# Kernel optimization log

Measured on AMD Instinct MI355X. Metric: run time of the kernel, lower is better.

The kernel has to match this reference:

```python
import jax, jax.numpy as jnp
import numpy as np

N_HEAD = 16
LORA_SCALE = 1.0 / 4.0  # alpha=1, r=4
LN_EPS = 1e-5


def _ln(x, g, b):
    # LayerNorm subclass casts to float32 then back to input dtype
    xf = x.astype(jnp.float32)
    m = xf.mean(-1, keepdims=True)
    v = xf.var(-1, keepdims=True)
    y = (xf - m) / jnp.sqrt(v + LN_EPS) * g + b
    return y.astype(x.dtype)


def _lora(h, a, b):
    # x @ a.T @ b.T * scaling ; a:[r,d], b:[d,r]
    return (h @ a.T) @ b.T * LORA_SCALE


def _attn(h, Wq, bq, Wk, Wv, bv, Wo, bo, la_k, lb_k, la_v, lb_v, la_o, lb_o):
    B, S, D = h.shape
    hd = D // N_HEAD
    scale = hd ** (-0.25)
    q = h @ Wq.T + bq
    k = h @ Wk.T + _lora(h, la_k, lb_k)          # key Linear has no bias
    v = h @ Wv.T + bv + _lora(h, la_v, lb_v)
    qh = q.reshape(B, S, N_HEAD, hd).transpose(0, 2, 1, 3) * scale  # [B,H,S,hd]
    kh = k.reshape(B, S, N_HEAD, hd).transpose(0, 2, 1, 3) * scale
    vh = v.reshape(B, S, N_HEAD, hd).transpose(0, 2, 1, 3)
    qk = jnp.einsum('bhqd,bhkd->bhqk', qh, kh).astype(jnp.float32)
    w = jax.nn.softmax(qk, axis=-1).astype(q.dtype)
    wv = jnp.einsum('bhqk,bhkd->bhqd', w, vh)
    wv = wv.transpose(0, 2, 1, 3).reshape(B, S, D)
    return wv @ Wo.T + bo + _lora(wv, la_o, lb_o)


def setup_inputs() -> dict:
    key = jax.random.key(0)
    D, R = 1024, 4
    B, S = 8, 1024
    ks = jax.random.split(key, 20)
    sd = 0.02
    inp = {
        'x': jax.random.normal(ks[0], (B, S, D), jnp.float32),
        'Wq': jax.random.normal(ks[1], (D, D), jnp.float32) * sd,
        'bq': jnp.zeros((D,), jnp.float32),
        'Wk': jax.random.normal(ks[2], (D, D), jnp.float32) * sd,
        'Wv': jax.random.normal(ks[3], (D, D), jnp.float32) * sd,
        'bv': jnp.zeros((D,), jnp.float32),
        'Wo': jax.random.normal(ks[4], (D, D), jnp.float32) * sd,
        'bo': jnp.zeros((D,), jnp.float32),
        'la_k': jax.random.normal(ks[5], (R, D), jnp.float32) * sd,
        'lb_k': jax.random.normal(ks[6], (D, R), jnp.float32) * sd,
        'la_v': jax.random.normal(ks[7], (R, D), jnp.float32) * sd,
        'lb_v': jax.random.normal(ks[8], (D, R), jnp.float32) * sd,
        'la_o': jax.random.normal(ks[9], (R, D), jnp.float32) * sd,
        'lb_o': jax.random.normal(ks[10], (D, R), jnp.float32) * sd,
        'g_attn': jnp.ones((D,), jnp.float32),
        'b_attn': jnp.zeros((D,), jnp.float32),
        'W1': jax.random.normal(ks[11], (4 * D, D), jnp.float32) * sd,
        'b1': jnp.zeros((4 * D,), jnp.float32),
        'W2': jax.random.normal(ks[12], (D, 4 * D), jnp.float32) * sd,
        'b2': jnp.zeros((D,), jnp.float32),
        'g_mlp': jnp.ones((D,), jnp.float32),
        'b_mlp': jnp.zeros((D,), jnp.float32),
    }
    return inp


def reference(x, Wq, bq, Wk, Wv, bv, Wo, bo, la_k, lb_k, la_v, lb_v, la_o, lb_o,
              g_attn, b_attn, W1, b1, W2, b2, g_mlp, b_mlp):
    # self-attention + residual (LoRA on key/value/out)
    x = x + _attn(_ln(x, g_attn, b_attn), Wq, bq, Wk, Wv, bv, Wo, bo,
                  la_k, lb_k, la_v, lb_v, la_o, lb_o)
    # MLP + residual (exact GELU, matching nn.GELU default)
    h = _ln(x, g_mlp, b_mlp)
    h = jax.nn.gelu(h @ W1.T + b1, approximate=False)
    x = x + h @ W2.T + b2
    return x
```

## Files before the change

kernel.cpp:

```cpp
#include <hip/hip_runtime.h>
#include <math.h>

typedef _Float16 f16_t;
typedef f16_t f16x8 __attribute__((ext_vector_type(8)));
typedef f16_t f16x4 __attribute__((ext_vector_type(4)));
typedef float f32x4 __attribute__((ext_vector_type(4)));
typedef float fv4 __attribute__((ext_vector_type(4)));

#define MFMA16(a, b, c) __builtin_amdgcn_mfma_f32_16x16x32_f16(a, b, c, 0, 0, 0)

__device__ __forceinline__ void gload16(const void* g, void* l) {
  __builtin_amdgcn_global_load_lds((const __attribute__((address_space(1))) void*)g,
                                   (__attribute__((address_space(3))) void*)l, 16, 0, 0);
}

__global__ __launch_bounds__(256) void ln_f32(const float* __restrict__ x,
                                              const float* __restrict__ g,
                                              const float* __restrict__ b,
                                              f16_t* __restrict__ y) {
  const int D = 1024;
  int row = blockIdx.x;
  int t = threadIdx.x;
  const float* xr = x + (size_t)row * D + t * 4;
  float x0 = xr[0], x1 = xr[1], x2 = xr[2], x3 = xr[3];
  float sum = x0 + x1 + x2 + x3;
  float sq = x0 * x0 + x1 * x1 + x2 * x2 + x3 * x3;
  for (int d = 32; d; d >>= 1) {
    sum += __shfl_down(sum, d);
    sq += __shfl_down(sq, d);
  }
  __shared__ float ssum[4], ssq[4];
  int w = t >> 6, lane = t & 63;
  if (lane == 0) { ssum[w] = sum; ssq[w] = sq; }
  __syncthreads();
  float ts = ssum[0] + ssum[1] + ssum[2] + ssum[3];
  float tq = ssq[0] + ssq[1] + ssq[2] + ssq[3];
  float mean = ts * (1.0f / 1024.0f);
  float var = tq * (1.0f / 1024.0f) - mean * mean;
  float rstd = rsqrtf(var + 1e-5f);
  f16_t* yr = y + (size_t)row * D + t * 4;
  const float* gr = g + t * 4;
  const float* br = b + t * 4;
  yr[0] = (f16_t)((x0 - mean) * rstd * gr[0] + br[0]);
  yr[1] = (f16_t)((x1 - mean) * rstd * gr[1] + br[1]);
  yr[2] = (f16_t)((x2 - mean) * rstd * gr[2] + br[2]);
  yr[3] = (f16_t)((x3 - mean) * rstd * gr[3] + br[3]);
}

__global__ __launch_bounds__(256) void ln_f16(const f16_t* __restrict__ x,
                                              const float* __restrict__ g,
                                              const float* __restrict__ b,
                                              f16_t* __restrict__ y) {
  const int D = 1024;
  int row = blockIdx.x;
  int t = threadIdx.x;
  const f16_t* xr = x + (size_t)row * D + t * 4;
  float x0 = (float)xr[0], x1 = (float)xr[1], x2 = (float)xr[2], x3 = (float)xr[3];
  float sum = x0 + x1 + x2 + x3;
  float sq = x0 * x0 + x1 * x1 + x2 * x2 + x3 * x3;
  for (int d = 32; d; d >>= 1) {
    sum += __shfl_down(sum, d);
    sq += __shfl_down(sq, d);
  }
  __shared__ float ssum[4], ssq[4];
  int w = t >> 6, lane = t & 63;
  if (lane == 0) { ssum[w] = sum; ssq[w] = sq; }
  __syncthreads();
  float ts = ssum[0] + ssum[1] + ssum[2] + ssum[3];
  float tq = ssq[0] + ssq[1] + ssq[2] + ssq[3];
  float mean = ts * (1.0f / 1024.0f);
  float var = tq * (1.0f / 1024.0f) - mean * mean;
  float rstd = rsqrtf(var + 1e-5f);
  f16_t* yr = y + (size_t)row * D + t * 4;
  const float* gr = g + t * 4;
  const float* br = b + t * 4;
  yr[0] = (f16_t)((x0 - mean) * rstd * gr[0] + br[0]);
  yr[1] = (f16_t)((x1 - mean) * rstd * gr[1] + br[1]);
  yr[2] = (f16_t)((x2 - mean) * rstd * gr[2] + br[2]);
  yr[3] = (f16_t)((x3 - mean) * rstd * gr[3] + br[3]);
}

__global__ __launch_bounds__(256) void convert_w(
    const float* __restrict__ wq, const float* __restrict__ wk,
    const float* __restrict__ wv, const float* __restrict__ wo,
    const float* __restrict__ w1, const float* __restrict__ w2,
    f16_t* __restrict__ oq, f16_t* __restrict__ ok, f16_t* __restrict__ ov,
    f16_t* __restrict__ oo, f16_t* __restrict__ o1, f16_t* __restrict__ o2) {
  int bid = blockIdx.x;
  const float* src;
  f16_t* dst;
  int bi;
  if (bid < 2048) {
    int seg = bid >> 9;
    bi = bid & 511;
    src = seg == 0 ? wq : seg == 1 ? wk : seg == 2 ? wv : wo;
    dst = seg == 0 ? oq : seg == 1 ? ok : seg == 2 ? ov : oo;
  } else if (bid < 4096) {
    bi = bid - 2048; src = w1; dst = o1;
  } else {
    bi = bid - 4096; src = w2; dst = o2;
  }
  size_t idx = (size_t)bi * 2048 + (size_t)threadIdx.x * 8;
  fv4 a = *(const fv4*)(src + idx);
  fv4 b = *(const fv4*)(src + idx + 4);
  f16x8 h;
#pragma unroll
  for (int j = 0; j < 4; ++j) { h[j] = (f16_t)a[j]; h[4 + j] = (f16_t)b[j]; }
  *(f16x8*)(dst + idx) = h;
}

__global__ __launch_bounds__(256) void lora_kv_kernel(
    const f16_t* __restrict__ h, const float* __restrict__ la_k,
    const float* __restrict__ la_v, float* __restrict__ t_k,
    float* __restrict__ t_v, int K) {
  int lane = threadIdx.x & 63;
  int w = threadIdx.x >> 6;
  int row = blockIdx.x * 4 + w;
  const f16_t* hrow = h + (size_t)row * K;
  float ak[4] = {0.f, 0.f, 0.f, 0.f};
  float av[4] = {0.f, 0.f, 0.f, 0.f};
  for (int it = 0; it < K / 512; ++it) {
    int base = it * 512 + lane * 8;
    f16x8 hx = *(const f16x8*)(hrow + base);
#pragma unroll
    for (int r = 0; r < 4; ++r) {
      const float* kr = la_k + (size_t)r * K + base;
      const float* vr = la_v + (size_t)r * K + base;
#pragma unroll
      for (int j = 0; j < 8; ++j) {
        float hv = (float)hx[j];
        ak[r] += hv * kr[j];
        av[r] += hv * vr[j];
      }
    }
  }
#pragma unroll
  for (int r = 0; r < 4; ++r) {
    for (int d = 32; d; d >>= 1) {
      ak[r] += __shfl_down(ak[r], d);
      av[r] += __shfl_down(av[r], d);
    }
  }
  if (lane == 0) {
#pragma unroll
    for (int r = 0; r < 4; ++r) {
      t_k[(size_t)row * 4 + r] = ak[r];
      t_v[(size_t)row * 4 + r] = av[r];
    }
  }
}

__global__ __launch_bounds__(256) void lora_t_kernel(const f16_t* __restrict__ h,
                                                     const float* __restrict__ la,
                                                     float* __restrict__ t, int K) {
  int lane = threadIdx.x & 63;
  int w = threadIdx.x >> 6;
  int row = blockIdx.x * 4 + w;
  const f16_t* hrow = h + (size_t)row * K;
  float acc[4] = {0.f, 0.f, 0.f, 0.f};
  for (int it = 0; it < K / 512; ++it) {
    int base = it * 512 + lane * 8;
    f16x8 hx = *(const f16x8*)(hrow + base);
#pragma unroll
    for (int r = 0; r < 4; ++r) {
      const float* ar = la + (size_t)r * K + base;
#pragma unroll
      for (int j = 0; j < 8; ++j) acc[r] += (float)hx[j] * ar[j];
    }
  }
#pragma unroll
  for (int r = 0; r < 4; ++r) {
    for (int d = 32; d; d >>= 1) acc[r] += __shfl_down(acc[r], d);
  }
  if (lane == 0) {
#pragma unroll
    for (int r = 0; r < 4; ++r) t[(size_t)row * 4 + r] = acc[r];
  }
}

#define GEMM_PIPE_BODY                                                        \
  f32x4 acc[4][4];                                                            \
  _Pragma("unroll") for (int i = 0; i < 4; ++i)                               \
      _Pragma("unroll") for (int j = 0; j < 4; ++j)                           \
          acc[i][j] = (f32x4){0.f, 0.f, 0.f, 0.f};                            \
  const int nsteps = K >> 6;                                                  \
  stageA(0, 0); stageB(0, 0);                                                 \
  stageA(1, 1); stageB(1, 1);                                                 \
  stageA(2, 2); stageB(2, 2);                                                 \
  int b3 = 0;                                                                 \
  for (int kt = 0; kt < nsteps; ++kt) {                                       \
    if (kt + 2 < nsteps)                                                      \
      asm volatile("s_waitcnt vmcnt(12)" ::: "memory");                       \
    else if (kt + 1 < nsteps)                                                 \
      asm volatile("s_waitcnt vmcnt(6)" ::: "memory");                        \
    else                                                                      \
      asm volatile("s_waitcnt vmcnt(0)" ::: "memory");                        \
    __builtin_amdgcn_sched_barrier(0);                                        \
    __builtin_amdgcn_s_barrier();                                             \
    f16x8 af[4][2], bf[4][2];                                                 \
    _Pragma("unroll") for (int kk = 0; kk < 2; ++kk) {                        \
      _Pragma("unroll") for (int i = 0; i < 4; ++i) {                         \
        int row = wm * 64 + i * 16 + l15;                                     \
        af[i][kk] = *(const f16x8*)((const char*)Abuf[b3] + row * 128 +       \
                                    ((kk * 64 + lhi * 16) ^ ((row & 7) << 4)));\
      }                                                                       \
      _Pragma("unroll") for (int j = 0; j < 4; ++j) {                         \
        int row = wn * 64 + j * 16 + l15;                                     \
        bf[j][kk] = *(const f16x8*)((const char*)Bbuf[b3] + row * 128 +       \
                                    ((kk * 64 + lhi * 16) ^ ((row & 7) << 4)));\
      }                                                                       \
    }                                                                         \
    asm volatile("s_waitcnt lgkmcnt(0)" ::: "memory");                        \
    __builtin_amdgcn_sched_barrier(0);                                        \
    __builtin_amdgcn_s_barrier();                                             \
    if (kt + 3 < nsteps) { stageA(kt + 3, b3); stageB(kt + 3, b3); }          \
    __builtin_amdgcn_sched_barrier(0);                                        \
    __builtin_amdgcn_s_setprio(1);                                            \
    _Pragma("unroll") for (int kk = 0; kk < 2; ++kk)                          \
        _Pragma("unroll") for (int i = 0; i < 4; ++i)                         \
            _Pragma("unroll") for (int j = 0; j < 4; ++j)                     \
                acc[i][j] = MFMA16(af[i][kk], bf[j][kk], acc[i][j]);          \
    __builtin_amdgcn_s_setprio(0);                                            \
    b3 = (b3 == 2) ? 0 : b3 + 1;                                              \
  }

__global__ __launch_bounds__(512, 2) void gemm_pipe(
    const f16_t* __restrict__ A, const f16_t* __restrict__ B,
    const float* __restrict__ bias, const float* __restrict__ loraT,
    const float* __restrict__ loraB, const float* residf,
    const f16_t* __restrict__ residb, f16_t* Cb, float* Cf,
    int M, int N, int K, int ldb, int dogelu) {
  __shared__ __align__(16) f16_t Abuf[3][8192];
  __shared__ __align__(16) f16_t Bbuf[3][16384];
  const int tid = threadIdx.x;
  const int lane = tid & 63, wid = tid >> 6;
  const int wm = wid >> 2, wn = wid & 3;
  const int l15 = lane & 15, lhi = lane >> 4;
  int nwg = gridDim.x * gridDim.y;
  int bid = blockIdx.y * gridDim.x + blockIdx.x;
  int swz = (bid & 7) * (nwg >> 3) + (bid >> 3);
  const int m0 = (swz / gridDim.x) * 128, n0 = (swz % gridDim.x) * 256;
  const int arow = tid >> 3;
  const int aslot = tid & 7;

  auto stageA = [&](int step, int buf) {
#pragma unroll
    for (int c = 0; c < 2; ++c) {
      int r = c * 64 + arow;
      int cm = aslot ^ (r & 7);
      gload16(A + (size_t)(m0 + r) * K + (size_t)step * 64 + cm * 8,
              (char*)Abuf[buf] + c * 8192 + wid * 1024);
    }
  };
  auto stageB = [&](int step, int buf) {
#pragma unroll
    for (int c = 0; c < 4; ++c) {
      int r = c * 64 + arow;
      int cm = aslot ^ (r & 7);
      gload16(B + (size_t)(n0 + r) * ldb + (size_t)step * 64 + cm * 8,
              (char*)Bbuf[buf] + c * 8192 + wid * 1024);
    }
  };

  GEMM_PIPE_BODY

  const int gm = m0 + wm * 64, gn = n0 + wn * 64;
#pragma unroll
  for (int j = 0; j < 4; ++j) {
    int gcol = gn + j * 16 + l15;
    float bj = bias ? bias[gcol] : 0.f;
    float lb0 = 0.f, lb1 = 0.f, lb2 = 0.f, lb3 = 0.f;
    if (loraB) {
      const float* p = loraB + (size_t)gcol * 4;
      lb0 = p[0]; lb1 = p[1]; lb2 = p[2]; lb3 = p[3];
    }
#pragma unroll
    for (int i = 0; i < 4; ++i) {
      float v4[4];
#pragma unroll
      for (int r = 0; r < 4; ++r) {
        int grow = gm + i * 16 + lhi * 4 + r;
        float val = acc[i][j][r] + bj;
        if (loraT) {
          const float* tp = loraT + (size_t)grow * 4;
          val += 0.25f * (tp[0] * lb0 + tp[1] * lb1 + tp[2] * lb2 + tp[3] * lb3);
        }
        if (dogelu) val = 0.5f * val * (1.0f + erff(val * 0.70710678118654752f));
        if (residf) val += residf[(size_t)grow * N + gcol];
        if (residb) val += (float)residb[(size_t)grow * N + gcol];
        v4[r] = val;
      }
      if (Cf) {
#pragma unroll
        for (int r = 0; r < 4; ++r)
          Cf[(size_t)(gm + i * 16 + lhi * 4 + r) * N + gcol] = v4[r];
      } else {
#pragma unroll
        for (int r = 0; r < 4; ++r)
          Cb[(size_t)(gm + i * 16 + lhi * 4 + r) * N + gcol] = (f16_t)v4[r];
      }
    }
  }
}

__global__ __launch_bounds__(512, 2) void gemm_qkv_pipe(
    const f16_t* __restrict__ A, const f16_t* __restrict__ W,
    const float* __restrict__ bq, const float* __restrict__ bv,
    const float* __restrict__ t_k, const float* __restrict__ lb_k,
    const float* __restrict__ t_v, const float* __restrict__ lb_v,
    f16_t* __restrict__ Pq, f16_t* __restrict__ Pk, f16_t* __restrict__ Pvt,
    int K) {
  const int D = 1024;
  __shared__ __align__(16) f16_t Abuf[3][8192];
  __shared__ __align__(16) f16_t Bbuf[3][16384];
  const int tid = threadIdx.x;
  const int lane = tid & 63, wid = tid >> 6;
  const int wm = wid >> 2, wn = wid & 3;
  const int l15 = lane & 15, lhi = lane >> 4;
  int nwg = gridDim.x * gridDim.y;
  int bid = blockIdx.y * gridDim.x + blockIdx.x;
  int swz = (bid & 7) * (nwg >> 3) + (bid >> 3);
  const int m0 = (swz / gridDim.x) * 128, n0 = (swz % gridDim.x) * 256;
  const int seg = n0 >> 10;
  const int arow = tid >> 3;
  const int aslot = tid & 7;

  auto stageA = [&](int step, int buf) {
#pragma unroll
    for (int c = 0; c < 2; ++c) {
      int r = c * 64 + arow;
      int cm = aslot ^ (r & 7);
      gload16(A + (size_t)(m0 + r) * K + (size_t)step * 64 + cm * 8,
              (char*)Abuf[buf] + c * 8192 + wid * 1024);
    }
  };
  auto stageB = [&](int step, int buf) {
#pragma unroll
    for (int c = 0; c < 4; ++c) {
      int r = c * 64 + arow;
      int cm = aslot ^ (r & 7);
      gload16(W + (size_t)(n0 + r) * K + (size_t)step * 64 + cm * 8,
              (char*)Bbuf[buf] + c * 8192 + wid * 1024);
    }
  };

  GEMM_PIPE_BODY

  const int gm = m0 + wm * 64, gn = n0 + wn * 64;
  const float* tB = (seg == 1) ? t_k : t_v;
#pragma unroll
  for (int j = 0; j < 4; ++j) {
    int gcol = gn + j * 16 + l15;
    int c = gcol & 1023;
    float bj = (seg == 0) ? bq[c] : (seg == 2 ? bv[c] : 0.f);
    float lb0 = 0.f, lb1 = 0.f, lb2 = 0.f, lb3 = 0.f;
    if (seg) {
      const float* p = (seg == 1 ? lb_k : lb_v) + (size_t)c * 4;
      lb0 = p[0]; lb1 = p[1]; lb2 = p[2]; lb3 = p[3];
    }
#pragma unroll
    for (int i = 0; i < 4; ++i) {
      float v4[4];
#pragma unroll
      for (int r = 0; r < 4; ++r) {
        int grow = gm + i * 16 + lhi * 4 + r;
        float val = acc[i][j][r] + bj;
        if (seg) {
          const float* tp = tB + (size_t)grow * 4;
          val += 0.25f * (tp[0] * lb0 + tp[1] * lb1 + tp[2] * lb2 + tp[3] * lb3);
        }
        v4[r] = val;
      }
      if (seg < 2) {
        f16_t* dst = (seg == 0) ? Pq : Pk;
#pragma unroll
        for (int r = 0; r < 4; ++r)
          dst[(size_t)(gm + i * 16 + lhi * 4 + r) * D + c] = (f16_t)v4[r];
      } else {
        int grow0 = gm + i * 16 + lhi * 4;
        int bb = grow0 >> 10, ss = grow0 & 1023;
        int hh = c >> 6, dd = c & 63;
        f16x4 pk;
#pragma unroll
        for (int r = 0; r < 4; ++r) pk[r] = (f16_t)v4[r];
        *(f16x4*)(Pvt + (((size_t)bb * 16 + hh) * 64 + dd) * 1024 + ss) = pk;
      }
    }
  }
}

__global__ __launch_bounds__(256, 2) void gemm_mfma(
    const f16_t* __restrict__ A, const float* __restrict__ B,
    const float* __restrict__ bias, const float* __restrict__ loraT,
    const float* __restrict__ loraB, const float* residf,
    const f16_t* __restrict__ residb, f16_t* Cb, float* Cf, f16_t* Cvt,
    int M, int N, int K, int ldb, int dogelu) {
  __shared__ __align__(16) f16_t smem[2][16384];
  const int tid = threadIdx.x;
  const int lane = tid & 63, wid = tid >> 6;
  const int wm = wid >> 1, wn = wid & 1;
  const int l15 = lane & 15, lhi = lane >> 4;
  const int m0 = blockIdx.y * 128, n0 = blockIdx.x * 128;
  const int arow = tid >> 3;
  const int aslot = tid & 7;

  f32x4 acc[4][4];
#pragma unroll
  for (int i = 0; i < 4; ++i)
#pragma unroll
    for (int j = 0; j < 4; ++j) acc[i][j] = (f32x4){0.f, 0.f, 0.f, 0.f};

  fv4 breg[4][2];

  auto stageA = [&](int step, int buf) {
#pragma unroll
    for (int c = 0; c < 4; ++c) {
      int r = c * 32 + arow;
      int cm = aslot ^ (r & 7);
      gload16(A + (size_t)(m0 + r) * K + (size_t)step * 64 + cm * 8,
              (char*)&smem[buf][0] + c * 4096 + wid * 1024);
    }
  };
  auto loadB = [&](int step) {
#pragma unroll
    for (int c = 0; c < 4; ++c) {
      int r = c * 32 + arow;
      const float* gp = B + (size_t)(n0 + r) * ldb + (size_t)step * 64 + aslot * 8;
      breg[c][0] = *(const fv4*)gp;
      breg[c][1] = *(const fv4*)(gp + 4);
    }
  };
  auto writeB = [&](int buf) {
#pragma unroll
    for (int c = 0; c < 4; ++c) {
      int r = c * 32 + arow;
      f16x8 hh;
#pragma unroll
      for (int j = 0; j < 4; ++j) hh[j] = (f16_t)breg[c][0][j];
#pragma unroll
      for (int j = 0; j < 4; ++j) hh[4 + j] = (f16_t)breg[c][1][j];
      int boff = r * 128 + ((aslot * 16) ^ ((r & 7) << 4));
      *(f16x8*)((char*)&smem[buf][8192] + boff) = hh;
    }
  };

  const int nsteps = K >> 6;
  stageA(0, 0);
  loadB(0);
  writeB(0);
  __syncthreads();
  for (int t = 0; t < nsteps; ++t) {
    int cur = t & 1, nxt = cur ^ 1;
    if (t + 1 < nsteps) { stageA(t + 1, nxt); loadB(t + 1); }
    const char* As = (const char*)&smem[cur][0];
    const char* Bs = (const char*)&smem[cur][8192];
#pragma unroll
    for (int kk = 0; kk < 2; ++kk) {
      f16x8 af[4], bf[4];
#pragma unroll
      for (int i = 0; i < 4; ++i) {
        int row = wm * 64 + i * 16 + l15;
        af[i] = *(const f16x8*)(As + row * 128 + ((kk * 64 + lhi * 16) ^ ((row & 7) << 4)));
      }
#pragma unroll
      for (int j = 0; j < 4; ++j) {
        int row = wn * 64 + j * 16 + l15;
        bf[j] = *(const f16x8*)(Bs + row * 128 + ((kk * 64 + lhi * 16) ^ ((row & 7) << 4)));
      }
#pragma unroll
      for (int i = 0; i < 4; ++i)
#pragma unroll
        for (int j = 0; j < 4; ++j) acc[i][j] = MFMA16(af[i], bf[j], acc[i][j]);
    }
    if (t + 1 < nsteps) writeB(nxt);
    __syncthreads();
  }

  const int gm = m0 + wm * 64, gn = n0 + wn * 64;
#pragma unroll
  for (int j = 0; j < 4; ++j) {
    int gcol = gn + j * 16 + l15;
    float bj = bias ? bias[gcol] : 0.f;
    float lb0 = 0.f, lb1 = 0.f, lb2 = 0.f, lb3 = 0.f;
    if (loraB) {
      const float* p = loraB + (size_t)gcol * 4;
      lb0 = p[0]; lb1 = p[1]; lb2 = p[2]; lb3 = p[3];
    }
#pragma unroll
    for (int i = 0; i < 4; ++i) {
      float v4[4];
#pragma unroll
      for (int r = 0; r < 4; ++r) {
        int grow = gm + i * 16 + lhi * 4 + r;
        float val = acc[i][j][r] + bj;
        if (loraT) {
          const float* tp = loraT + (size_t)grow * 4;
          val += 0.25f * (tp[0] * lb0 + tp[1] * lb1 + tp[2] * lb2 + tp[3] * lb3);
        }
        if (dogelu) val = 0.5f * val * (1.0f + erff(val * 0.70710678118654752f));
        if (residf) val += residf[(size_t)grow * N + gcol];
        if (residb) val += (float)residb[(size_t)grow * N + gcol];
        v4[r] = val;
      }
      if (Cf) {
#pragma unroll
        for (int r = 0; r < 4; ++r)
          Cf[(size_t)(gm + i * 16 + lhi * 4 + r) * N + gcol] = v4[r];
      } else if (Cvt) {
        int grow0 = gm + i * 16 + lhi * 4;
        int bb = grow0 >> 10, ss = grow0 & 1023;
        int hh = gcol >> 6, dd = gcol & 63;
        f16x4 pk;
#pragma unroll
        for (int r = 0; r < 4; ++r) pk[r] = (f16_t)v4[r];
        *(f16x4*)(Cvt + (((size_t)bb * 16 + hh) * 64 + dd) * 1024 + ss) = pk;
      } else {
#pragma unroll
        for (int r = 0; r < 4; ++r)
          Cb[(size_t)(gm + i * 16 + lhi * 4 + r) * N + gcol] = (f16_t)v4[r];
      }
    }
  }
}

__global__ __launch_bounds__(256, 3) void attn_mfma(const f16_t* __restrict__ q,
                                                    const f16_t* __restrict__ k,
                                                    const f16_t* __restrict__ vt,
                                                    f16_t* __restrict__ wv) {
  const int S = 1024, D = 1024;
  __shared__ __align__(16) f16_t Qs[128 * 64];
  __shared__ __align__(16) f16_t SP[128 * 64];
  __shared__ __align__(16) f16_t Ks[64 * 64];
  __shared__ __align__(16) f16_t Vts[64 * 64];
  __shared__ float rsb[128];
  __shared__ float lib[128];
  const int tid = threadIdx.x, lane = tid & 63, w = tid >> 6;
  const int l15 = lane & 15, lhi = lane >> 4;
  const int q0 = blockIdx.x * 128;
  const int h = blockIdx.y, b = blockIdx.z;
  const f16_t* qg = q + ((size_t)b * S + q0) * D + h * 64;
  const f16_t* kg = k + (size_t)b * S * D + h * 64;
  const f16_t* vg = vt + ((size_t)b * 16 + h) * 64 * (size_t)S;

#pragma unroll
  for (int c = 0; c < 4; ++c) {
    int r = c * 32 + (tid >> 3), kc = tid & 7;
    f16x8 xx = *(const f16x8*)(qg + (size_t)r * D + kc * 8);
    *(f16x8*)((char*)Qs + r * 128 + ((kc * 16) ^ ((r & 7) << 4))) = xx;
  }
  __syncthreads();
  f16x8 qf[2][2];
#pragma unroll
  for (int i = 0; i < 2; ++i) {
    int row = w * 32 + i * 16 + l15;
#pragma unroll
    for (int kk = 0; kk < 2; ++kk)
      qf[i][kk] = *(const f16x8*)((char*)Qs + row * 128 +
                                  ((kk * 64 + lhi * 16) ^ ((row & 7) << 4)));
  }

  f32x4 oacc[2][4];
#pragma unroll
  for (int i = 0; i < 2; ++i)
#pragma unroll
    for (int j = 0; j < 4; ++j) oacc[i][j] = (f32x4){0.f, 0.f, 0.f, 0.f};
  float m_run = -1e30f, l_run = 0.f;
  const int myrow = w * 32 + (lane >> 1);
  const int half = lane & 1;

  for (int kv = 0; kv < 16; ++kv) {
    __syncthreads();
#pragma unroll
    for (int c = 0; c < 2; ++c) {
      int r = c * 32 + (tid >> 3), kc = tid & 7;
      f16x8 xk = *(const f16x8*)(kg + (size_t)(kv * 64 + r) * D + kc * 8);
      *(f16x8*)((char*)Ks + r * 128 + ((kc * 16) ^ ((r & 7) << 4))) = xk;
      f16x8 xv = *(const f16x8*)(vg + (size_t)r * S + kv * 64 + kc * 8);
      *(f16x8*)((char*)Vts + r * 128 + ((kc * 16) ^ ((r & 7) << 4))) = xv;
    }
    __syncthreads();
    f32x4 sacc[2][4];
#pragma unroll
    for (int i = 0; i < 2; ++i)
#pragma unroll
      for (int j = 0; j < 4; ++j) sacc[i][j] = (f32x4){0.f, 0.f, 0.f, 0.f};
#pragma unroll
    for (int kk = 0; kk < 2; ++kk) {
      f16x8 kf[4];
#pragma unroll
      for (int j = 0; j < 4; ++j) {
        int row = j * 16 + l15;
        kf[j] = *(const f16x8*)((char*)Ks + row * 128 +
                                ((kk * 64 + lhi * 16) ^ ((row & 7) << 4)));
      }
#pragma unroll
      for (int i = 0; i < 2; ++i)
#pragma unroll
        for (int j = 0; j < 4; ++j) sacc[i][j] = MFMA16(qf[i][kk], kf[j], sacc[i][j]);
    }
#pragma unroll
    for (int i = 0; i < 2; ++i)
#pragma unroll
      for (int j = 0; j < 4; ++j)
#pragma unroll
        for (int r = 0; r < 4; ++r) {
          int srow = w * 32 + i * 16 + lhi * 4 + r;
          int scol = j * 16 + l15;
          *(f16_t*)((char*)SP + srow * 128 + ((scol * 2) ^ ((srow & 7) << 4))) =
              (f16_t)(sacc[i][j][r] * 0.125f);
        }
    __syncthreads();
    f16x8 ch[4];
#pragma unroll
    for (int c = 0; c < 4; ++c)
      ch[c] = *(const f16x8*)((char*)SP + myrow * 128 +
                              ((half * 64 + c * 16) ^ ((myrow & 7) << 4)));
    float mt = -1e30f;
#pragma unroll
    for (int c = 0; c < 4; ++c)
#pragma unroll
      for (int e = 0; e < 8; ++e) mt = fmaxf(mt, (float)ch[c][e]);
    mt = fmaxf(mt, __shfl_xor(mt, 1));
    float mnew = fmaxf(m_run, mt);
    float resc = __expf(m_run - mnew);
    float lsum = 0.f;
#pragma unroll
    for (int c = 0; c < 4; ++c) {
      f16x8 p8;
#pragma unroll
      for (int e = 0; e < 8; ++e) {
        float p = __expf((float)ch[c][e] - mnew);
        lsum += p;
        p8[e] = (f16_t)p;
      }
      *(f16x8*)((char*)SP + myrow * 128 + ((half * 64 + c * 16) ^ ((myrow & 7) << 4))) = p8;
    }
    lsum += __shfl_xor(lsum, 1);
    l_run = l_run * resc + lsum;
    m_run = mnew;
    if (half == 0) rsb[myrow] = resc;
    __syncthreads();
#pragma unroll
    for (int i = 0; i < 2; ++i) {
      float f0 = rsb[w * 32 + i * 16 + lhi * 4 + 0];
      float f1 = rsb[w * 32 + i * 16 + lhi * 4 + 1];
      float f2 = rsb[w * 32 + i * 16 + lhi * 4 + 2];
      float f3 = rsb[w * 32 + i * 16 + lhi * 4 + 3];
#pragma unroll
      for (int j = 0; j < 4; ++j) {
        oacc[i][j][0] *= f0;
        oacc[i][j][1] *= f1;
        oacc[i][j][2] *= f2;
        oacc[i][j][3] *= f3;
      }
    }
#pragma unroll
    for (int kk = 0; kk < 2; ++kk) {
      f16x8 pa[2], vb[4];
#pragma unroll
      for (int i = 0; i < 2; ++i) {
        int row = w * 32 + i * 16 + l15;
        pa[i] = *(const f16x8*)((char*)SP + row * 128 +
                                ((kk * 64 + lhi * 16) ^ ((row & 7) << 4)));
      }
#pragma unroll
      for (int j = 0; j < 4; ++j) {
        int row = j * 16 + l15;
        vb[j] = *(const f16x8*)((char*)Vts + row * 128 +
                                ((kk * 64 + lhi * 16) ^ ((row & 7) << 4)));
      }
#pragma unroll
      for (int i = 0; i < 2; ++i)
#pragma unroll
        for (int j = 0; j < 4; ++j) oacc[i][j] = MFMA16(pa[i], vb[j], oacc[i][j]);
    }
  }
  if (half == 0) lib[myrow] = 1.f / l_run;
  __syncthreads();
#pragma unroll
  for (int i = 0; i < 2; ++i)
#pragma unroll
    for (int r = 0; r < 4; ++r) {
      int row = w * 32 + i * 16 + lhi * 4 + r;
      float li = lib[row];
      size_t base = ((size_t)b * S + q0 + row) * D + h * 64;
#pragma unroll
      for (int j = 0; j < 4; ++j)
        wv[base + j * 16 + l15] = (f16_t)(oacc[i][j][r] * li);
    }
}

extern "C" void kernel_launch(void* const* d_in, const int* in_sizes, int n_in,
                              void* d_out, int out_size, void* d_ws, size_t ws_size,
                              hipStream_t stream) {
  const int B = 8, S = 1024, D = 1024, F = 4096;
  const int M = B * S;

  const float* x = (const float*)d_in[0];
  const float* Wq = (const float*)d_in[1];
  const float* bq = (const float*)d_in[2];
  const float* Wk = (const float*)d_in[3];
  const float* Wv = (const float*)d_in[4];
  const float* bv = (const float*)d_in[5];
  const float* Wo = (const float*)d_in[6];
  const float* bo = (const float*)d_in[7];
  const float* la_k = (const float*)d_in[8];
  const float* lb_k = (const float*)d_in[9];
  const float* la_v = (const float*)d_in[10];
  const float* lb_v = (const float*)d_in[11];
  const float* la_o = (const float*)d_in[12];
  const float* lb_o = (const float*)d_in[13];
  const float* g_attn = (const float*)d_in[14];
  const float* b_attn = (const float*)d_in[15];
  const float* W1 = (const float*)d_in[16];
  const float* b1 = (const float*)d_in[17];
  const float* W2 = (const float*)d_in[18];
  const float* b2 = (const float*)d_in[19];
  const float* g_mlp = (const float*)d_in[20];
  const float* b_mlp = (const float*)d_in[21];

  float* t_k = (float*)((char*)d_ws + 16);
  float* t_v = t_k + (size_t)M * 4;
  float* t_o = t_v + (size_t)M * 4;
  const size_t MD = (size_t)M * D;
  f16_t* P0 = (f16_t*)((char*)d_ws + 409600);
  f16_t* P1 = P0 + MD;
  f16_t* P2 = P0 + 2 * MD;
  f16_t* P3 = P0 + 3 * MD;
  f16_t* Wqkvf = P0 + 4 * MD;
  f16_t* Wof = Wqkvf + 3 * (size_t)D * D;
  f16_t* W1f = Wof + (size_t)D * D;
  f16_t* W2f = W1f + (size_t)F * D;
  float* outf = (float*)d_out;
  const size_t need = 409600 + 4 * MD * sizeof(f16_t) +
                      (4 * (size_t)D * D + 2 * (size_t)F * D) * sizeof(f16_t);
  const bool f16w = ws_size >= need;

  if (f16w)
    convert_w<<<6144, 256, 0, stream>>>(
        Wq, Wk, Wv, Wo, W1, W2, Wqkvf, Wqkvf + (size_t)D * D,
        Wqkvf + 2 * (size_t)D * D, Wof, W1f, W2f);

  ln_f32<<<M, 256, 0, stream>>>(x, g_attn, b_attn, P0);
  lora_kv_kernel<<<M / 4, 256, 0, stream>>>(P0, la_k, la_v, t_k, t_v, D);
  if (f16w) {
    gemm_qkv_pipe<<<dim3(12, 64), 512, 0, stream>>>(
        P0, Wqkvf, bq, bv, t_k, lb_k, t_v, lb_v, P1, P2, P3, D);
  } else {
    gemm_mfma<<<dim3(8, 64), 256, 0, stream>>>(
        P0, Wq, bq, nullptr, nullptr, nullptr, nullptr, P1, nullptr, nullptr,
        M, D, D, D, 0);
    gemm_mfma<<<dim3(8, 64), 256, 0, stream>>>(
        P0, Wk, nullptr, t_k, lb_k, nullptr, nullptr, P2, nullptr, nullptr,
        M, D, D, D, 0);
    gemm_mfma<<<dim3(8, 64), 256, 0, stream>>>(
        P0, Wv, bv, t_v, lb_v, nullptr, nullptr, nullptr, nullptr, P3,
        M, D, D, D, 0);
  }
  attn_mfma<<<dim3(8, 16, 8), 256, 0, stream>>>(P1, P2, P3, P0);
  lora_t_kernel<<<M / 4, 256, 0, stream>>>(P0, la_o, t_o, D);
  if (f16w)
    gemm_pipe<<<dim3(4, 64), 512, 0, stream>>>(
        P0, Wof, bo, t_o, lb_o, x, nullptr, P3, nullptr, M, D, D, D, 0);
  else
    gemm_mfma<<<dim3(8, 64), 256, 0, stream>>>(
        P0, Wo, bo, t_o, lb_o, x, nullptr, P3, nullptr, nullptr, M, D, D, D, 0);
  ln_f16<<<M, 256, 0, stream>>>(P3, g_mlp, b_mlp, P0);
  if (f16w) {
    gemm_pipe<<<dim3(8, 64), 512, 0, stream>>>(
        P0, W1f, b1, nullptr, nullptr, nullptr, nullptr, P1, nullptr,
        M, 2048, D, D, 1);
    gemm_pipe<<<dim3(4, 64), 512, 0, stream>>>(
        P1, W2f, b2, nullptr, nullptr, nullptr, P3, nullptr, outf,
        M, D, 2048, F, 0);
    gemm_pipe<<<dim3(8, 64), 512, 0, stream>>>(
        P0, W1f + (size_t)2048 * D, b1 + 2048, nullptr, nullptr, nullptr, nullptr,
        P1, nullptr, M, 2048, D, D, 1);
    gemm_pipe<<<dim3(4, 64), 512, 0, stream>>>(
        P1, W2f + 2048, nullptr, nullptr, nullptr, outf, nullptr, nullptr, outf,
        M, D, 2048, F, 0);
  } else {
    gemm_mfma<<<dim3(16, 64), 256, 0, stream>>>(
        P0, W1, b1, nullptr, nullptr, nullptr, nullptr, P1, nullptr, nullptr,
        M, 2048, D, D, 1);
    gemm_mfma<<<dim3(8, 64), 256, 0, stream>>>(
        P1, W2, b2, nullptr, nullptr, nullptr, P3, nullptr, outf, nullptr,
        M, D, 2048, F, 0);
    gemm_mfma<<<dim3(16, 64), 256, 0, stream>>>(
        P0, W1 + (size_t)2048 * D, b1 + 2048, nullptr, nullptr, nullptr, nullptr,
        P1, nullptr, nullptr, M, 2048, D, D, 1);
    gemm_mfma<<<dim3(8, 64), 256, 0, stream>>>(
        P1, W2 + 2048, nullptr, nullptr, nullptr, outf, nullptr, nullptr, outf,
        nullptr, M, D, 2048, F, 0);
  }
}
```

Baseline: 646.7 us.

## Fuse LoRA K/V down-projection into LayerNorm; enlarge attention blocks to 256 queries

Merges the key/value LoRA down-projection into the first LayerNorm kernel, so the normalized row is dotted with la_k/la_v while still in registers. This removes one launch and a re-read of the f16 activations, and it uses the f32 LN values instead of f16-rounded ones. The attention kernel now runs 512 threads over 256 query rows per block, reusing the shared K/V tiles for twice as many queries and reusing the P buffer for the Q staging to save LDS. The risks are fewer blocks (512 total) and a higher occupancy target from launch bounds (512,6) that may pressure registers.

New measurement: 859.2 us. 1.33x slower.

```diff
diff --git a/kernel.cpp b/kernel.cpp
--- a/kernel.cpp
+++ b/kernel.cpp
@@ -14,10 +14,11 @@
                                    (__attribute__((address_space(3))) void*)l, 16, 0, 0);
 }
 
-__global__ __launch_bounds__(256) void ln_f32(const float* __restrict__ x,
-                                              const float* __restrict__ g,
-                                              const float* __restrict__ b,
-                                              f16_t* __restrict__ y) {
+__global__ __launch_bounds__(256) void ln_lora_f32(
+    const float* __restrict__ x, const float* __restrict__ g,
+    const float* __restrict__ b, const float* __restrict__ la_k,
+    const float* __restrict__ la_v, f16_t* __restrict__ y,
+    float* __restrict__ t_k, float* __restrict__ t_v) {
   const int D = 1024;
   int row = blockIdx.x;
   int t = threadIdx.x;
@@ -30,6 +31,7 @@
     sq += __shfl_down(sq, d);
   }
   __shared__ float ssum[4], ssq[4];
+  __shared__ float red[4][8];
   int w = t >> 6, lane = t & 63;
   if (lane == 0) { ssum[w] = sum; ssq[w] = sq; }
   __syncthreads();
@@ -38,13 +40,35 @@
   float mean = ts * (1.0f / 1024.0f);
   float var = tq * (1.0f / 1024.0f) - mean * mean;
   float rstd = rsqrtf(var + 1e-5f);
-  f16_t* yr = y + (size_t)row * D + t * 4;
   const float* gr = g + t * 4;
   const float* br = b + t * 4;
-  yr[0] = (f16_t)((x0 - mean) * rstd * gr[0] + br[0]);
-  yr[1] = (f16_t)((x1 - mean) * rstd * gr[1] + br[1]);
-  yr[2] = (f16_t)((x2 - mean) * rstd * gr[2] + br[2]);
-  yr[3] = (f16_t)((x3 - mean) * rstd * gr[3] + br[3]);
+  float y0 = (x0 - mean) * rstd * gr[0] + br[0];
+  float y1 = (x1 - mean) * rstd * gr[1] + br[1];
+  float y2 = (x2 - mean) * rstd * gr[2] + br[2];
+  float y3 = (x3 - mean) * rstd * gr[3] + br[3];
+  f16_t* yr = y + (size_t)row * D + t * 4;
+  yr[0] = (f16_t)y0; yr[1] = (f16_t)y1; yr[2] = (f16_t)y2; yr[3] = (f16_t)y3;
+  float a[8];
+#pragma unroll
+  for (int r = 0; r < 4; ++r) {
+    const float* kr = la_k + (size_t)r * D + t * 4;
+    const float* vr = la_v + (size_t)r * D + t * 4;
+    a[r] = y0 * kr[0] + y1 * kr[1] + y2 * kr[2] + y3 * kr[3];
+    a[4 + r] = y0 * vr[0] + y1 * vr[1] + y2 * vr[2] + y3 * vr[3];
+  }
+#pragma unroll
+  for (int i = 0; i < 8; ++i)
+    for (int d = 32; d; d >>= 1) a[i] += __shfl_down(a[i], d);
+  if (lane == 0) {
+#pragma unroll
+    for (int i = 0; i < 8; ++i) red[w][i] = a[i];
+  }
+  __syncthreads();
+  if (t < 8) {
+    float s = red[0][t] + red[1][t] + red[2][t] + red[3][t];
+    if (t < 4) t_k[(size_t)row * 4 + t] = s;
+    else t_v[(size_t)row * 4 + (t - 4)] = s;
+  }
 }
 
 __global__ __launch_bounds__(256) void ln_f16(const f16_t* __restrict__ x,
@@ -107,47 +131,6 @@
 #pragma unroll
   for (int j = 0; j < 4; ++j) { h[j] = (f16_t)a[j]; h[4 + j] = (f16_t)b[j]; }
   *(f16x8*)(dst + idx) = h;
-}
-
-__global__ __launch_bounds__(256) void lora_kv_kernel(
-    const f16_t* __restrict__ h, const float* __restrict__ la_k,
-    const float* __restrict__ la_v, float* __restrict__ t_k,
-    float* __restrict__ t_v, int K) {
-  int lane = threadIdx.x & 63;
-  int w = threadIdx.x >> 6;
-  int row = blockIdx.x * 4 + w;
-  const f16_t* hrow = h + (size_t)row * K;
-  float ak[4] = {0.f, 0.f, 0.f, 0.f};
-  float av[4] = {0.f, 0.f, 0.f, 0.f};
-  for (int it = 0; it < K / 512; ++it) {
-    int base = it * 512 + lane * 8;
-    f16x8 hx = *(const f16x8*)(hrow + base);
-#pragma unroll
-    for (int r = 0; r < 4; ++r) {
-      const float* kr = la_k + (size_t)r * K + base;
-      const float* vr = la_v + (size_t)r * K + base;
-#pragma unroll
-      for (int j = 0; j < 8; ++j) {
-        float hv = (float)hx[j];
-        ak[r] += hv * kr[j];
-        av[r] += hv * vr[j];
-      }
-    }
-  }
-#pragma unroll
-  for (int r = 0; r < 4; ++r) {
-    for (int d = 32; d; d >>= 1) {
-      ak[r] += __shfl_down(ak[r], d);
-      av[r] += __shfl_down(av[r], d);
-    }
-  }
-  if (lane == 0) {
-#pragma unroll
-    for (int r = 0; r < 4; ++r) {
-      t_k[(size_t)row * 4 + r] = ak[r];
-      t_v[(size_t)row * 4 + r] = av[r];
-    }
-  }
 }
 
 __global__ __launch_bounds__(256) void lora_t_kernel(const f16_t* __restrict__ h,
@@ -523,20 +506,19 @@
   }
 }
 
-__global__ __launch_bounds__(256, 3) void attn_mfma(const f16_t* __restrict__ q,
+__global__ __launch_bounds__(512, 6) void attn_mfma(const f16_t* __restrict__ q,
                                                     const f16_t* __restrict__ k,
                                                     const f16_t* __restrict__ vt,
                                                     f16_t* __restrict__ wv) {
   const int S = 1024, D = 1024;
-  __shared__ __align__(16) f16_t Qs[128 * 64];
-  __shared__ __align__(16) f16_t SP[128 * 64];
+  __shared__ __align__(16) f16_t SP[256 * 64];
   __shared__ __align__(16) f16_t Ks[64 * 64];
   __shared__ __align__(16) f16_t Vts[64 * 64];
-  __shared__ float rsb[128];
-  __shared__ float lib[128];
+  __shared__ float rsb[256];
+  __shared__ float lib[256];
   const int tid = threadIdx.x, lane = tid & 63, w = tid >> 6;
   const int l15 = lane & 15, lhi = lane >> 4;
-  const int q0 = blockIdx.x * 128;
+  const int q0 = blockIdx.x * 256;
   const int h = blockIdx.y, b = blockIdx.z;
   const f16_t* qg = q + ((size_t)b * S + q0) * D + h * 64;
   const f16_t* kg = k + (size_t)b * S * D + h * 64;
@@ -544,9 +526,10 @@
 
 #pragma unroll
   for (int c = 0; c < 4; ++c) {
-    int r = c * 32 + (tid >> 3), kc = tid & 7;
+    int idx = c * 512 + tid;
+    int r = idx >> 3, kc = idx & 7;
     f16x8 xx = *(const f16x8*)(qg + (size_t)r * D + kc * 8);
-    *(f16x8*)((char*)Qs + r * 128 + ((kc * 16) ^ ((r & 7) << 4))) = xx;
+    *(f16x8*)((char*)SP + r * 128 + ((kc * 16) ^ ((r & 7) << 4))) = xx;
   }
   __syncthreads();
   f16x8 qf[2][2];
@@ -555,7 +538,7 @@
     int row = w * 32 + i * 16 + l15;
 #pragma unroll
     for (int kk = 0; kk < 2; ++kk)
-      qf[i][kk] = *(const f16x8*)((char*)Qs + row * 128 +
+      qf[i][kk] = *(const f16x8*)((char*)SP + row * 128 +
                                   ((kk * 64 + lhi * 16) ^ ((row & 7) << 4)));
   }
 
@@ -570,9 +553,8 @@
 
   for (int kv = 0; kv < 16; ++kv) {
     __syncthreads();
-#pragma unroll
-    for (int c = 0; c < 2; ++c) {
-      int r = c * 32 + (tid >> 3), kc = tid & 7;
+    {
+      int r = tid >> 3, kc = tid & 7;
       f16x8 xk = *(const f16x8*)(kg + (size_t)(kv * 64 + r) * D + kc * 8);
       *(f16x8*)((char*)Ks + r * 128 + ((kc * 16) ^ ((r & 7) << 4))) = xk;
       f16x8 xv = *(const f16x8*)(vg + (size_t)r * S + kv * 64 + kc * 8);
@@ -741,8 +723,7 @@
         Wq, Wk, Wv, Wo, W1, W2, Wqkvf, Wqkvf + (size_t)D * D,
         Wqkvf + 2 * (size_t)D * D, Wof, W1f, W2f);
 
-  ln_f32<<<M, 256, 0, stream>>>(x, g_attn, b_attn, P0);
-  lora_kv_kernel<<<M / 4, 256, 0, stream>>>(P0, la_k, la_v, t_k, t_v, D);
+  ln_lora_f32<<<M, 256, 0, stream>>>(x, g_attn, b_attn, la_k, la_v, P0, t_k, t_v);
   if (f16w) {
     gemm_qkv_pipe<<<dim3(12, 64), 512, 0, stream>>>(
         P0, Wqkvf, bq, bv, t_k, lb_k, t_v, lb_v, P1, P2, P3, D);
@@ -757,7 +738,7 @@
         P0, Wv, bv, t_v, lb_v, nullptr, nullptr, nullptr, nullptr, P3,
         M, D, D, D, 0);
   }
-  attn_mfma<<<dim3(8, 16, 8), 256, 0, stream>>>(P1, P2, P3, P0);
+  attn_mfma<<<dim3(4, 16, 8), 512, 0, stream>>>(P1, P2, P3, P0);
   lora_t_kernel<<<M / 4, 256, 0, stream>>>(P0, la_o, t_o, D);
   if (f16w)
     gemm_pipe<<<dim3(4, 64), 512, 0, stream>>>(
```
